# Performance work log

Hardware: AMD Instinct MI355X
Metric: run time of the kernel (lower is better)

## Reference

```python
import jax, jax.numpy as jnp
import numpy as np
import math

B_SZ, T, D_IN, D_OUT, N = 8, 4096, 256, 256, 512
RMIN, RMAX, MAX_PHASE = 0.99, 1.0, 6.283


def setup_inputs() -> dict:
    key = jax.random.key(0)
    ks = jax.random.split(key, 8)
    u_in = jax.random.normal(ks[0], (B_SZ, T, D_IN), dtype=jnp.float32)
    u1 = jax.random.uniform(ks[1], (N,), dtype=jnp.float32)
    u2 = jax.random.uniform(ks[2], (N,), dtype=jnp.float32)
    # LRU parametrization from 'Resurrecting Linear Recurrences'
    nu_log = jnp.log(-0.5 * jnp.log(u1 * (RMAX + RMIN) * (RMAX - RMIN) + RMIN ** 2))
    theta_log = jnp.log(MAX_PHASE * u2)
    lambda_mod = jnp.exp(-jnp.exp(nu_log))
    gamma_log = jnp.log(jnp.sqrt(1.0 - jnp.square(lambda_mod)))
    B_real = jax.random.normal(ks[3], (N, D_IN), dtype=jnp.float32) / math.sqrt(2 * D_IN)
    B_imag = jax.random.normal(ks[4], (N, D_IN), dtype=jnp.float32) / math.sqrt(2 * D_IN)
    C_real = jax.random.normal(ks[5], (D_OUT, N), dtype=jnp.float32) / math.sqrt(N)
    C_imag = jax.random.normal(ks[6], (D_OUT, N), dtype=jnp.float32) / math.sqrt(N)
    D = jax.random.normal(ks[7], (D_OUT, D_IN), dtype=jnp.float32) / math.sqrt(D_IN)
    return {"u_in": u_in, "nu_log": nu_log, "theta_log": theta_log,
            "gamma_log": gamma_log, "B_real": B_real, "B_imag": B_imag,
            "C_real": C_real, "C_imag": C_imag, "D": D}


def _lru_forward(u_in, nu_log, theta_log, gamma_log, B_real, B_imag, C_real, C_imag, D):
    lambda_mod = jnp.exp(-jnp.exp(nu_log))
    theta = jnp.exp(theta_log)
    lam = (lambda_mod * jnp.cos(theta) + 1j * lambda_mod * jnp.sin(theta)).astype(jnp.complex64)  # [N]
    gammas = jnp.exp(gamma_log)
    Bc = (B_real + 1j * B_imag).astype(jnp.complex64)  # [N, D_in]
    Cc = (C_real + 1j * C_imag).astype(jnp.complex64)  # [D_out, N]
    # driving term: gamma * (u_t @ B^T)  -> [b, t, n]
    Bu = gammas.astype(jnp.complex64) * jnp.einsum('bti,ni->btn', u_in.astype(jnp.complex64), Bc)
    # linear recurrence x_t = lam * x_{t-1} + Bu_t, x_0 prior = 0, via associative scan
    a = jnp.broadcast_to(lam, Bu.shape)

    def combine(e1, e2):
        a1, b1 = e1
        a2, b2 = e2
        return a1 * a2, a2 * b1 + b2

    _, x = jax.lax.associative_scan(combine, (a, Bu), axis=1)  # [b, t, n] complex
    y = 2.0 * jnp.real(jnp.einsum('btn,on->bto', x, Cc)) + jnp.einsum('bti,oi->bto', u_in, D)
    return y


def reference(u_in, nu_log, theta_log, gamma_log, B_real, B_imag, C_real, C_imag, D):
    return _lru_forward(u_in, nu_log, theta_log, gamma_log, B_real, B_imag, C_real, C_imag, D)
```

## Files before the change

### kernel.cpp

```cpp
#include <hip/hip_runtime.h>
#include <hip/hip_bf16.h>
#include <math.h>

#define B_SZ    8
#define T_LEN   4096
#define DIN     256
#define DOUT    256
#define NST     512
#define M_ROWS  (B_SZ * T_LEN)
#define N1      (2 * NST)
#define K2      (N1 + DIN)
#define CHL     128
#define NCH     (T_LEN / CHL)

typedef __attribute__((ext_vector_type(8))) short bf16x8;
typedef __attribute__((ext_vector_type(4))) float f32x4;
typedef __hip_bfloat16 bf16;

#define OFF_UBF  67108864
#define OFF_WP   83886080
#define OFF_W2   84410368
#define OFF_LAM  85065728
#define OFF_LAML 85069824
#define OFF_SSUM 85073920

__device__ __forceinline__ void gl_lds16(const bf16* g, bf16* l) {
    __builtin_amdgcn_global_load_lds(
        (const __attribute__((address_space(1))) void*)g,
        (__attribute__((address_space(3))) void*)l, 16, 0, 0);
}

__global__ __launch_bounds__(256) void prep(const float* __restrict__ u,
        const float* __restrict__ nu_log, const float* __restrict__ theta_log,
        const float* __restrict__ gamma_log,
        const float* __restrict__ B_real, const float* __restrict__ B_imag,
        const float* __restrict__ C_real, const float* __restrict__ C_imag,
        const float* __restrict__ Dm,
        bf16* __restrict__ ub, bf16* __restrict__ Wp, bf16* __restrict__ W2,
        float* __restrict__ lam, float* __restrict__ lamL) {
    int bid = blockIdx.x, tid = threadIdx.x;
    if (bid < 8192) {
        int i = bid * 256 + tid;
        float4 v = ((const float4*)u)[i];
        union { bf16 h[4]; uint2 u2; } p;
        p.h[0] = __float2bfloat16(v.x); p.h[1] = __float2bfloat16(v.y);
        p.h[2] = __float2bfloat16(v.z); p.h[3] = __float2bfloat16(v.w);
        ((uint2*)ub)[i] = p.u2;
    } else if (bid < 9216) {
        int c = bid - 8192;
        int n = c & (NST - 1);
        float g = expf(gamma_log[n]);
        const float* src = (c < NST) ? (B_real + (size_t)n * DIN)
                                     : (B_imag + (size_t)n * DIN);
        Wp[(size_t)c * DIN + tid] = __float2bfloat16(g * src[tid]);
        int idx = c * 256 + tid;
        if (idx < NST) {
            float lm = expf(-expf(nu_log[idx]));
            float th = expf(theta_log[idx]);
            float lr = lm * cosf(th), li = lm * sinf(th);
            lam[idx] = lr; lam[NST + idx] = li;
            float ar = lr, ai = li;
#pragma unroll
            for (int q = 0; q < 7; ++q) {
                float nr = ar * ar - ai * ai;
                float ni = 2.f * ar * ai;
                ar = nr; ai = ni;
            }
            lamL[idx] = ar; lamL[NST + idx] = ai;
        }
    } else {
        int idx = (bid - 9216) * 256 + tid;
        if (idx < DOUT * K2) {
            int o = idx / K2, c = idx - o * K2;
            float v;
            if (c < NST)            v =  2.0f * C_real[(size_t)o * NST + c];
            else if (c < 2 * NST)   v = -2.0f * C_imag[(size_t)o * NST + (c - NST)];
            else                    v =  Dm[(size_t)o * DIN + (c - 2 * NST)];
            W2[idx] = __float2bfloat16(v);
        }
    }
}

__global__ __launch_bounds__(256) void gemm1(const bf16* __restrict__ u,
                                             const bf16* __restrict__ Wp,
                                             bf16* __restrict__ Bu) {
    __shared__ bf16 As[128 * 32];
    __shared__ bf16 Bs[128 * 32];
    __shared__ bf16 Cs[128 * 136];
    const int tid = threadIdx.x;
    const int m0 = blockIdx.x * 128, n0 = blockIdx.y * 128;
    const int lane = tid & 63, w = tid >> 6;
    const int wm = (w >> 1) * 64, wn = (w & 1) * 64;
    const int lr16 = lane & 15, kq = (lane >> 4) * 8;
    const int srow = tid >> 2, scol = (tid & 3) * 8;

    f32x4 acc[4][4] = {};
    for (int k0 = 0; k0 < DIN; k0 += 32) {
        gl_lds16(u  + (size_t)(m0 + srow) * DIN + k0 + scol,       &As[tid * 8]);
        gl_lds16(u  + (size_t)(m0 + 64 + srow) * DIN + k0 + scol,  &As[2048 + tid * 8]);
        gl_lds16(Wp + (size_t)(n0 + srow) * DIN + k0 + scol,       &Bs[tid * 8]);
        gl_lds16(Wp + (size_t)(n0 + 64 + srow) * DIN + k0 + scol,  &Bs[2048 + tid * 8]);
        __syncthreads();
        bf16x8 af[4], bfr[4];
#pragma unroll
        for (int i = 0; i < 4; ++i)
            af[i] = *(const bf16x8*)(&As[(wm + i * 16 + lr16) * 32 + kq]);
#pragma unroll
        for (int j = 0; j < 4; ++j)
            bfr[j] = *(const bf16x8*)(&Bs[(wn + j * 16 + lr16) * 32 + kq]);
#pragma unroll
        for (int i = 0; i < 4; ++i)
#pragma unroll
            for (int j = 0; j < 4; ++j)
                acc[i][j] = __builtin_amdgcn_mfma_f32_16x16x32_bf16(af[i], bfr[j], acc[i][j], 0, 0, 0);
        __syncthreads();
    }
    const int crow = (lane >> 4) * 4, ccol = lane & 15;
#pragma unroll
    for (int i = 0; i < 4; ++i)
#pragma unroll
        for (int j = 0; j < 4; ++j)
#pragma unroll
            for (int r = 0; r < 4; ++r)
                Cs[(wm + i * 16 + crow + r) * 136 + wn + j * 16 + ccol] =
                    __float2bfloat16(acc[i][j][r]);
    __syncthreads();
#pragma unroll
    for (int p = 0; p < 8; ++p) {
        int row = p * 16 + (tid >> 4);
        int colg = (tid & 15) * 8;
        *(uint4*)(&Bu[(size_t)(m0 + row) * N1 + n0 + colg]) =
            *(const uint4*)(&Cs[row * 136 + colg]);
    }
}

__global__ __launch_bounds__(512) void scan1(const bf16* __restrict__ Bu,
                                             const float* __restrict__ lam,
                                             float* __restrict__ Ssum) {
    int n = threadIdx.x;
    int c = blockIdx.x;
    int b = blockIdx.y;
    float lr = lam[n], li = lam[NST + n];
    const bf16* base = Bu + ((size_t)b * T_LEN + (size_t)c * CHL) * N1;
    float sr = 0.f, si = 0.f;
    for (int j = 0; j < CHL; ++j) {
        float br = __bfloat162float(base[(size_t)j * N1 + n]);
        float bi = __bfloat162float(base[(size_t)j * N1 + NST + n]);
        float tr = lr * sr - li * si + br;
        float ti = lr * si + li * sr + bi;
        sr = tr; si = ti;
    }
    size_t o = ((size_t)b * NCH + c) * N1 + n;
    Ssum[o] = sr; Ssum[o + NST] = si;
}

__global__ __launch_bounds__(512) void scan3(bf16* __restrict__ Bu,
                                             const float* __restrict__ lam,
                                             const float* __restrict__ lamL,
                                             const float* __restrict__ Ssum) {
    int n = threadIdx.x, c = blockIdx.x, b = blockIdx.y;
    float lr = lam[n], li = lam[NST + n];
    float Lr = lamL[n], Li = lamL[NST + n];
    float pr = 0.f, pi = 0.f;
    for (int cp = 0; cp < c; ++cp) {
        size_t o = ((size_t)b * NCH + cp) * N1 + n;
        float sr = Ssum[o], si = Ssum[o + NST];
        float tr = Lr * pr - Li * pi + sr;
        float ti = Lr * pi + Li * pr + si;
        pr = tr; pi = ti;
    }
    float xr = pr, xi = pi;
    bf16* base = Bu + ((size_t)b * T_LEN + (size_t)c * CHL) * N1;
    for (int j = 0; j < CHL; ++j) {
        float br = __bfloat162float(base[(size_t)j * N1 + n]);
        float bi = __bfloat162float(base[(size_t)j * N1 + NST + n]);
        float tr = lr * xr - li * xi + br;
        float ti = lr * xi + li * xr + bi;
        xr = tr; xi = ti;
        base[(size_t)j * N1 + n]       = __float2bfloat16(xr);
        base[(size_t)j * N1 + NST + n] = __float2bfloat16(xi);
    }
}

__global__ __launch_bounds__(512) void gemm2(const bf16* __restrict__ X,
                                             const bf16* __restrict__ u,
                                             const bf16* __restrict__ W2,
                                             float* __restrict__ y) {
    __shared__ bf16 As[128 * 32];
    __shared__ bf16 Bs[128 * 32];
    const int tid = threadIdx.x;
    const int m0 = blockIdx.x * 128, n0 = blockIdx.y * 128;
    const int lane = tid & 63, w = tid >> 6;
    const int wm = (w >> 2) * 64, wn = (w & 3) * 32;
    const int lr16 = lane & 15, kq = (lane >> 4) * 8;
    const int srow = tid >> 2, scol = (tid & 3) * 8;

    f32x4 acc[4][2] = {};
    for (int k0 = 0; k0 < K2; k0 += 32) {
        const bf16* Asrc; size_t lda; int kc;
        if (k0 < N1) { Asrc = X; lda = N1;  kc = k0; }
        else         { Asrc = u; lda = DIN; kc = k0 - N1; }
        gl_lds16(Asrc + (size_t)(m0 + srow) * lda + kc + scol, &As[tid * 8]);
        gl_lds16(W2 + (size_t)(n0 + srow) * K2 + k0 + scol,    &Bs[tid * 8]);
        __syncthreads();
        bf16x8 af[4], bfr[2];
#pragma unroll
        for (int i = 0; i < 4; ++i)
            af[i] = *(const bf16x8*)(&As[(wm + i * 16 + lr16) * 32 + kq]);
#pragma unroll
        for (int j = 0; j < 2; ++j)
            bfr[j] = *(const bf16x8*)(&Bs[(wn + j * 16 + lr16) * 32 + kq]);
#pragma unroll
        for (int i = 0; i < 4; ++i)
#pragma unroll
            for (int j = 0; j < 2; ++j)
                acc[i][j] = __builtin_amdgcn_mfma_f32_16x16x32_bf16(af[i], bfr[j], acc[i][j], 0, 0, 0);
        __syncthreads();
    }
    const int crow = (lane >> 4) * 4, ccol = lane & 15;
#pragma unroll
    for (int i = 0; i < 4; ++i)
#pragma unroll
        for (int j = 0; j < 2; ++j)
#pragma unroll
            for (int r = 0; r < 4; ++r)
                y[(size_t)(m0 + wm + i * 16 + crow + r) * DOUT + n0 + wn + j * 16 + ccol] = acc[i][j][r];
}

extern "C" void kernel_launch(void* const* d_in, const int* in_sizes, int n_in,
                              void* d_out, int out_size, void* d_ws, size_t ws_size,
                              hipStream_t stream) {
    const float* u_in      = (const float*)d_in[0];
    const float* nu_log    = (const float*)d_in[1];
    const float* theta_log = (const float*)d_in[2];
    const float* gamma_log = (const float*)d_in[3];
    const float* B_real    = (const float*)d_in[4];
    const float* B_imag    = (const float*)d_in[5];
    const float* C_real    = (const float*)d_in[6];
    const float* C_imag    = (const float*)d_in[7];
    const float* Dm        = (const float*)d_in[8];
    float* y = (float*)d_out;
    char* ws = (char*)d_ws;

    bf16*  Bu   = (bf16*)ws;
    bf16*  u_bf = (bf16*)(ws + OFF_UBF);
    bf16*  Wp   = (bf16*)(ws + OFF_WP);
    bf16*  W2   = (bf16*)(ws + OFF_W2);
    float* lam  = (float*)(ws + OFF_LAM);
    float* lamL = (float*)(ws + OFF_LAML);
    float* Ssum = (float*)(ws + OFF_SSUM);

    prep<<<10496, 256, 0, stream>>>(u_in, nu_log, theta_log, gamma_log,
                                    B_real, B_imag, C_real, C_imag, Dm,
                                    u_bf, Wp, W2, lam, lamL);
    gemm1<<<dim3(M_ROWS / 128, N1 / 128), 256, 0, stream>>>(u_bf, Wp, Bu);
    scan1<<<dim3(NCH, B_SZ), 512, 0, stream>>>(Bu, lam, Ssum);
    scan3<<<dim3(NCH, B_SZ), 512, 0, stream>>>(Bu, lam, lamL, Ssum);
    gemm2<<<dim3(M_ROWS / 128, DOUT / 128), 512, 0, stream>>>(Bu, u_bf, W2, y);
}
```

Before: 199.0 us.

## Halve scan chunk length and process two states per thread with packed bf16

Reduces the chunk length of the chunked linear-recurrence scan so more blocks run concurrently with shorter serial chains, adjusting the precomputed lambda power accordingly. Each scan thread now handles two adjacent state channels with 32-bit packed bf16 loads/stores, halving block size. This aims to raise GPU occupancy and memory efficiency in the latency-bound scans, at the cost of a longer cross-chunk prefix loop and a larger chunk-sum buffer.

```diff
diff --git a/kernel.cpp b/kernel.cpp
--- a/kernel.cpp
+++ b/kernel.cpp
@@ -10,7 +10,7 @@
 #define M_ROWS  (B_SZ * T_LEN)
 #define N1      (2 * NST)
 #define K2      (N1 + DIN)
-#define CHL     128
+#define CHL     64
 #define NCH     (T_LEN / CHL)
 
 typedef __attribute__((ext_vector_type(8))) short bf16x8;
@@ -28,6 +28,17 @@
     __builtin_amdgcn_global_load_lds(
         (const __attribute__((address_space(1))) void*)g,
         (__attribute__((address_space(3))) void*)l, 16, 0, 0);
+}
+__device__ __forceinline__ float bf_lo(unsigned w) {
+    union { unsigned u; float f; } c; c.u = w << 16; return c.f;
+}
+__device__ __forceinline__ float bf_hi(unsigned w) {
+    union { unsigned u; float f; } c; c.u = w & 0xffff0000u; return c.f;
+}
+__device__ __forceinline__ unsigned bf_pack2(float a, float b) {
+    union { bf16 h[2]; unsigned u; } p;
+    p.h[0] = __float2bfloat16(a); p.h[1] = __float2bfloat16(b);
+    return p.u;
 }
 
 __global__ __launch_bounds__(256) void prep(const float* __restrict__ u,
@@ -61,7 +72,7 @@
             lam[idx] = lr; lam[NST + idx] = li;
             float ar = lr, ai = li;
 #pragma unroll
-            for (int q = 0; q < 7; ++q) {
+            for (int q = 0; q < 6; ++q) {
                 float nr = ar * ar - ai * ai;
                 float ni = 2.f * ar * ai;
                 ar = nr; ai = ni;
@@ -134,51 +145,62 @@
     }
 }
 
-__global__ __launch_bounds__(512) void scan1(const bf16* __restrict__ Bu,
+__global__ __launch_bounds__(256) void scan1(const bf16* __restrict__ Bu,
                                              const float* __restrict__ lam,
                                              float* __restrict__ Ssum) {
-    int n = threadIdx.x;
+    int i = threadIdx.x;
     int c = blockIdx.x;
     int b = blockIdx.y;
-    float lr = lam[n], li = lam[NST + n];
+    float2 lrp = *(const float2*)(lam + 2 * i);
+    float2 lip = *(const float2*)(lam + NST + 2 * i);
     const bf16* base = Bu + ((size_t)b * T_LEN + (size_t)c * CHL) * N1;
-    float sr = 0.f, si = 0.f;
+    float sr0 = 0.f, si0 = 0.f, sr1 = 0.f, si1 = 0.f;
     for (int j = 0; j < CHL; ++j) {
-        float br = __bfloat162float(base[(size_t)j * N1 + n]);
-        float bi = __bfloat162float(base[(size_t)j * N1 + NST + n]);
-        float tr = lr * sr - li * si + br;
-        float ti = lr * si + li * sr + bi;
-        sr = tr; si = ti;
-    }
-    size_t o = ((size_t)b * NCH + c) * N1 + n;
-    Ssum[o] = sr; Ssum[o + NST] = si;
-}
-
-__global__ __launch_bounds__(512) void scan3(bf16* __restrict__ Bu,
+        const unsigned* rp = (const unsigned*)(base + (size_t)j * N1);
+        unsigned wr = rp[i];
+        unsigned wi = rp[256 + i];
+        float br0 = bf_lo(wr), br1 = bf_hi(wr);
+        float bi0 = bf_lo(wi), bi1 = bf_hi(wi);
+        float t;
+        t = lrp.x * sr0 - lip.x * si0 + br0; si0 = lrp.x * si0 + lip.x * sr0 + bi0; sr0 = t;
+        t = lrp.y * sr1 - lip.y * si1 + br1; si1 = lrp.y * si1 + lip.y * sr1 + bi1; sr1 = t;
+    }
+    size_t o = ((size_t)b * NCH + c) * N1;
+    *(float2*)(Ssum + o + 2 * i)       = make_float2(sr0, sr1);
+    *(float2*)(Ssum + o + NST + 2 * i) = make_float2(si0, si1);
+}
+
+__global__ __launch_bounds__(256) void scan3(bf16* __restrict__ Bu,
                                              const float* __restrict__ lam,
                                              const float* __restrict__ lamL,
                                              const float* __restrict__ Ssum) {
-    int n = threadIdx.x, c = blockIdx.x, b = blockIdx.y;
-    float lr = lam[n], li = lam[NST + n];
-    float Lr = lamL[n], Li = lamL[NST + n];
-    float pr = 0.f, pi = 0.f;
+    int i = threadIdx.x, c = blockIdx.x, b = blockIdx.y;
+    float2 lrp = *(const float2*)(lam + 2 * i);
+    float2 lip = *(const float2*)(lam + NST + 2 * i);
+    float2 Lrp = *(const float2*)(lamL + 2 * i);
+    float2 Lip = *(const float2*)(lamL + NST + 2 * i);
+    float pr0 = 0.f, pi0 = 0.f, pr1 = 0.f, pi1 = 0.f;
     for (int cp = 0; cp < c; ++cp) {
-        size_t o = ((size_t)b * NCH + cp) * N1 + n;
-        float sr = Ssum[o], si = Ssum[o + NST];
-        float tr = Lr * pr - Li * pi + sr;
-        float ti = Lr * pi + Li * pr + si;
-        pr = tr; pi = ti;
-    }
-    float xr = pr, xi = pi;
+        size_t o = ((size_t)b * NCH + cp) * N1;
+        float2 s_r = *(const float2*)(Ssum + o + 2 * i);
+        float2 s_i = *(const float2*)(Ssum + o + NST + 2 * i);
+        float t;
+        t = Lrp.x * pr0 - Lip.x * pi0 + s_r.x; pi0 = Lrp.x * pi0 + Lip.x * pr0 + s_i.x; pr0 = t;
+        t = Lrp.y * pr1 - Lip.y * pi1 + s_r.y; pi1 = Lrp.y * pi1 + Lip.y * pr1 + s_i.y; pr1 = t;
+    }
+    float xr0 = pr0, xi0 = pi0, xr1 = pr1, xi1 = pi1;
     bf16* base = Bu + ((size_t)b * T_LEN + (size_t)c * CHL) * N1;
     for (int j = 0; j < CHL; ++j) {
-        float br = __bfloat162float(base[(size_t)j * N1 + n]);
-        float bi = __bfloat162float(base[(size_t)j * N1 + NST + n]);
-        float tr = lr * xr - li * xi + br;
-        float ti = lr * xi + li * xr + bi;
-        xr = tr; xi = ti;
-        base[(size_t)j * N1 + n]       = __float2bfloat16(xr);
-        base[(size_t)j * N1 + NST + n] = __float2bfloat16(xi);
+        unsigned* rp = (unsigned*)(base + (size_t)j * N1);
+        unsigned wr = rp[i];
+        unsigned wi = rp[256 + i];
+        float br0 = bf_lo(wr), br1 = bf_hi(wr);
+        float bi0 = bf_lo(wi), bi1 = bf_hi(wi);
+        float t;
+        t = lrp.x * xr0 - lip.x * xi0 + br0; xi0 = lrp.x * xi0 + lip.x * xr0 + bi0; xr0 = t;
+        t = lrp.y * xr1 - lip.y * xi1 + br1; xi1 = lrp.y * xi1 + lip.y * xr1 + bi1; xr1 = t;
+        rp[i]       = bf_pack2(xr0, xr1);
+        rp[256 + i] = bf_pack2(xi0, xi1);
     }
 }
 
@@ -254,7 +276,7 @@
                                     B_real, B_imag, C_real, C_imag, Dm,
                                     u_bf, Wp, W2, lam, lamL);
     gemm1<<<dim3(M_ROWS / 128, N1 / 128), 256, 0, stream>>>(u_bf, Wp, Bu);
-    scan1<<<dim3(NCH, B_SZ), 512, 0, stream>>>(Bu, lam, Ssum);
-    scan3<<<dim3(NCH, B_SZ), 512, 0, stream>>>(Bu, lam, lamL, Ssum);
+    scan1<<<dim3(NCH, B_SZ), 256, 0, stream>>>(Bu, lam, Ssum);
+    scan3<<<dim3(NCH, B_SZ), 256, 0, stream>>>(Bu, lam, lamL, Ssum);
     gemm2<<<dim3(M_ROWS / 128, DOUT / 128), 512, 0, stream>>>(Bu, u_bf, W2, y);
 }
```

Result: no change. 202.6 us (+1.8%).
